# Performance work log

Hardware: AMD Instinct MI355X
Metric: run time of the kernel (lower is better)

## Reference

```python
import jax, jax.numpy as jnp
import numpy as np

WINSIZE = 11
SIGMA = 1.5
L_RANGE = 1.0

def _gaussian_window(winsize, channel, dtype=jnp.float32):
    x = jnp.arange(winsize, dtype=dtype)
    g = jnp.exp(-((x - winsize // 2) ** 2) / (2.0 * SIGMA ** 2))
    g = g / g.sum()
    w2d = jnp.outer(g, g)                      # [ws, ws]
    # depthwise kernel [channel, 1, ws, ws] (OIHW, feature_group_count=channel)
    return jnp.broadcast_to(w2d, (channel, 1, winsize, winsize))

def _dwconv(x, w, channel):
    pad = WINSIZE // 2
    return jax.lax.conv_general_dilated(
        x, w, window_strides=(1, 1), padding=[(pad, pad), (pad, pad)],
        dimension_numbers=('NCHW', 'OIHW', 'NCHW'),
        feature_group_count=channel)

def _ssim(X, Y):
    channel = X.shape[1]
    w = _gaussian_window(WINSIZE, channel, X.dtype)
    mu1 = _dwconv(X, w, channel)
    mu2 = _dwconv(Y, w, channel)
    mu1_sq = mu1 * mu1
    mu2_sq = mu2 * mu2
    mu1_mu2 = mu1 * mu2
    sigma1_sq = _dwconv(X * X, w, channel) - mu1_sq
    sigma2_sq = _dwconv(Y * Y, w, channel) - mu2_sq
    sigma12 = _dwconv(X * Y, w, channel) - mu1_mu2
    C1 = (0.01 * L_RANGE) ** 2
    C2 = (0.03 * L_RANGE) ** 2
    ssim_map = ((2.0 * mu1_mu2 + C1) * (2.0 * sigma12 + C2)) / \
               ((mu1_sq + mu2_sq + C1) * (sigma1_sq + sigma2_sq + C2))
    return jnp.mean(ssim_map)  # sizeavg=True

def setup_inputs() -> dict:
    key = jax.random.key(0)
    k1, k2 = jax.random.split(key)
    shape = (16, 3, 512, 512)
    X = jax.random.uniform(k1, shape, dtype=jnp.float32)
    Y = jax.random.uniform(k2, shape, dtype=jnp.float32)
    return {"X": X, "Y": Y}

def reference(X, Y):
    return 1.0 - _ssim(X, Y)
```

## Files before the change

### kernel.cpp

```cpp
#include <hip/hip_runtime.h>
#include <hip/hip_fp16.h>


#define ROWS 32
#define NI   (ROWS + 10)
#define NSTRIP 3072
#define NBLK  (NSTRIP / 4)
#define NPIX  12582912.0

static __device__ __forceinline__ unsigned fun16(unsigned hi, unsigned lo) {
    return (unsigned)((((unsigned long long)hi << 32) | lo) >> 16);
}
static __device__ __forceinline__ unsigned h2u(__half2 v) {
    unsigned u; __builtin_memcpy(&u, &v, 4); return u;
}
static __device__ __forceinline__ __half2 u2h(unsigned u) {
    __half2 v; __builtin_memcpy(&v, &u, 4); return v;
}

__global__ __launch_bounds__(256, 3) void ssim_sweep_kernel(
    const float* __restrict__ X, const float* __restrict__ Y,
    float* __restrict__ partial)
{
    __shared__ unsigned sbw[4][2][2][72];

    const int tid  = threadIdx.x;
    const int lane = tid & 63;
    const int w    = tid >> 6;
    const int sid  = blockIdx.x * 4 + w;
    const int img  = sid >> 6;
    const int rb   = (sid >> 2) & 15;
    const int cs   = (sid & 3) << 7;
    const int r0   = rb * ROWS;

    const float* __restrict__ Xi = X + (size_t)img * (512 * 512);
    const float* __restrict__ Yi = Y + (size_t)img * (512 * 512);

    float g[11];
    {
        float s = 0.f;
        #pragma unroll
        for (int i = 0; i < 11; ++i) {
            float d = (float)(i - 5);
            float e = expf(-d * d * (1.0f / 4.5f));
            g[i] = e; s += e;
        }
        float inv = 1.0f / s;
        #pragma unroll
        for (int i = 0; i < 11; ++i) g[i] *= inv;
    }
    __half2 w2[11];
    #pragma unroll
    for (int i = 0; i < 11; ++i) w2[i] = __float2half2_rn(g[i]);

    const int c2 = cs + 2 * lane;

    int hq = -1, hm = 0;
    if (lane >= 48 && lane < 54)      { hq = lane - 48; hm = 0; }
    else if (lane >= 56 && lane < 62) { hq = lane - 56; hm = 1; }
    const int  hwd = (hq < 0) ? 0 : (hq < 3 ? hq : 64 + hq);
    const int  hc  = cs - 6 + 2 * hwd;
    const bool hok = (hq >= 0) && ((unsigned)hc < 512u);
    const float* hbase = hm ? Yi : Xi;

    float2 nvx, nvy, nvh;
    #define STAGE_LOAD(J)                                                    \
        {                                                                    \
            int gr = r0 - 5 + (J);                                           \
            nvx = make_float2(0.f, 0.f); nvy = nvx; nvh = nvx;               \
            if ((unsigned)gr < 512u) {                                       \
                const float* xr = Xi + (size_t)gr * 512;                     \
                const float* yr = Yi + (size_t)gr * 512;                     \
                nvx = *(const float2*)(xr + c2);                             \
                nvy = *(const float2*)(yr + c2);                             \
                if (hok) nvh = *(const float2*)(hbase + (size_t)gr * 512 + hc); \
            }                                                                \
        }
    #define STAGE_WRITE(BUF)                                                 \
        {                                                                    \
            sbw[w][0][BUF][3 + lane] = h2u(__floats2half2_rn(nvx.x, nvx.y)); \
            sbw[w][1][BUF][3 + lane] = h2u(__floats2half2_rn(nvy.x, nvy.y)); \
            if (hq >= 0) sbw[w][hm][BUF][hwd] = h2u(__floats2half2_rn(nvh.x, nvh.y)); \
        }

    STAGE_LOAD(0);
    STAGE_WRITE(0);
    asm volatile("s_waitcnt lgkmcnt(0)" ::: "memory");

    __half2 ring[5][11];
    float acc = 0.f;
    const float C1 = 1e-4f, C2 = 9e-4f;
    const __half2 hz = __float2half2_rn(0.f);

    #pragma unroll 1
    for (int jb = 0; jb < 44; jb += 11) {
        #pragma unroll
        for (int ph = 0; ph < 11; ++ph) {
            const int j = jb + ph;
            if (j < NI) {
                const int cur = j & 1, nxt = cur ^ 1;

                if (j + 1 < NI) STAGE_LOAD(j + 1);

                unsigned Dx[7], Dy[7];
                #pragma unroll
                for (int k2 = 0; k2 < 7; ++k2) Dx[k2] = sbw[w][0][cur][lane + k2];
                #pragma unroll
                for (int k2 = 0; k2 < 7; ++k2) Dy[k2] = sbw[w][1][cur][lane + k2];

                __half2 hx = hz, hy = hz, hxx = hz, hyy = hz, hxy = hz;
                #pragma unroll
                for (int k = 0; k < 11; ++k) {
                    unsigned ux, uy;
                    if (k & 1) { ux = Dx[(k + 1) >> 1];            uy = Dy[(k + 1) >> 1]; }
                    else       { ux = fun16(Dx[(k >> 1) + 1], Dx[k >> 1]);
                                 uy = fun16(Dy[(k >> 1) + 1], Dy[k >> 1]); }
                    __half2 xk = u2h(ux), yk = u2h(uy);
                    __half2 wx = __hmul2(w2[k], xk);
                    __half2 wy = __hmul2(w2[k], yk);
                    hx  = __hadd2(hx, wx);
                    hy  = __hadd2(hy, wy);
                    hxx = __hfma2(wx, xk, hxx);
                    hyy = __hfma2(wy, yk, hyy);
                    hxy = __hfma2(wx, yk, hxy);
                }
                ring[0][ph] = hx;  ring[1][ph] = hy;
                ring[2][ph] = hxx; ring[3][ph] = hyy; ring[4][ph] = hxy;

                if (j >= 10) {
                    __half2 mu1 = hz, mu2 = hz, vxx = hz, vyy = hz, vxy = hz;
                    #pragma unroll
                    for (int k = 0; k < 11; ++k) {
                        const int s = (ph + 1 + k) % 11;
                        mu1 = __hfma2(w2[k], ring[0][s], mu1);
                        mu2 = __hfma2(w2[k], ring[1][s], mu2);
                        vxx = __hfma2(w2[k], ring[2][s], vxx);
                        vyy = __hfma2(w2[k], ring[3][s], vyy);
                        vxy = __hfma2(w2[k], ring[4][s], vxy);
                    }
                    float2 m1 = __half22float2(mu1);
                    float2 m2 = __half22float2(mu2);
                    float2 xx = __half22float2(vxx);
                    float2 yy = __half22float2(vyy);
                    float2 xy = __half22float2(vxy);
                    #pragma unroll
                    for (int h = 0; h < 2; ++h) {
                        float a1 = h ? m1.y : m1.x;
                        float a2 = h ? m2.y : m2.x;
                        float bx = h ? xx.y : xx.x;
                        float by = h ? yy.y : yy.x;
                        float bz = h ? xy.y : xy.x;
                        float m11 = a1 * a1, m22 = a2 * a2, m12 = a1 * a2;
                        float s1 = bx - m11, s2 = by - m22, s12 = bz - m12;
                        float num = (2.f * m12 + C1) * (2.f * s12 + C2);
                        float den = (m11 + m22 + C1) * (s1 + s2 + C2);
                        acc = fmaf(num, __builtin_amdgcn_rcpf(den), acc);
                    }
                }

                if (j + 1 < NI) STAGE_WRITE(nxt);
                asm volatile("s_waitcnt lgkmcnt(0)" ::: "memory");
            }
        }
    }

    #pragma unroll
    for (int off = 32; off > 0; off >>= 1)
        acc += __shfl_down(acc, off, 64);
    if (lane == 0) partial[sid] = acc;
}

__global__ __launch_bounds__(256) void ssim_reduce_kernel(
    const float* __restrict__ partial, float* __restrict__ out)
{
    const int tid = threadIdx.x;
    double s = 0.0;
    for (int i = tid; i < NSTRIP; i += 256) s += (double)partial[i];
    __shared__ double sd[256];
    sd[tid] = s;
    __syncthreads();
    for (int off = 128; off > 0; off >>= 1) {
        if (tid < off) sd[tid] += sd[tid + off];
        __syncthreads();
    }
    if (tid == 0) out[0] = (float)(1.0 - sd[0] / NPIX);
}

extern "C" void kernel_launch(void* const* d_in, const int* in_sizes, int n_in,
                              void* d_out, int out_size, void* d_ws, size_t ws_size,
                              hipStream_t stream) {
    const float* X = (const float*)d_in[0];
    const float* Y = (const float*)d_in[1];
    float* partial = (float*)d_ws;
    float* out = (float*)d_out;

    ssim_sweep_kernel<<<NBLK, 256, 0, stream>>>(X, Y, partial);
    ssim_reduce_kernel<<<1, 256, 0, stream>>>(partial, out);
}
```

Baseline: 61.19 us.

## Swap conv order to vertical-then-horizontal with wave shuffles instead of LDS

The separable Gaussian now runs vertically first over an 11-row register ring of raw X/Y values. The horizontal pass uses cross-lane shuffles, so the shared-memory staging buffers, halo-loading lanes and LDS waits are gone. Each wave covers overlapping 116-column strips with 6-column halos on each side, and a per-lane mask drops halo outputs. Strips are shorter (16 rows), which raises the vertical halo overhead and the number of redundant loads. Five shuffle-based horizontal convolutions per output row replace the previous LDS reads.

```diff
diff --git a/kernel.cpp b/kernel.cpp
--- a/kernel.cpp
+++ b/kernel.cpp
@@ -2,11 +2,11 @@
 #include <hip/hip_fp16.h>
 
 
-#define ROWS 32
-#define NI   (ROWS + 10)
-#define NSTRIP 3072
-#define NBLK  (NSTRIP / 4)
-#define NPIX  12582912.0
+#define R      16
+#define NIT    (R + 10)
+#define NSTRIP (48 * 32 * 5)
+#define NBLK   (NSTRIP / 4)
+#define NPIX   12582912.0
 
 static __device__ __forceinline__ unsigned fun16(unsigned hi, unsigned lo) {
     return (unsigned)((((unsigned long long)hi << 32) | lo) >> 16);
@@ -18,34 +18,35 @@
     __half2 v; __builtin_memcpy(&v, &u, 4); return v;
 }
 
-__global__ __launch_bounds__(256, 3) void ssim_sweep_kernel(
+__global__ __launch_bounds__(256) void ssim_vh_kernel(
     const float* __restrict__ X, const float* __restrict__ Y,
     float* __restrict__ partial)
 {
-    __shared__ unsigned sbw[4][2][2][72];
-
     const int tid  = threadIdx.x;
     const int lane = tid & 63;
     const int w    = tid >> 6;
     const int sid  = blockIdx.x * 4 + w;
-    const int img  = sid >> 6;
-    const int rb   = (sid >> 2) & 15;
-    const int cs   = (sid & 3) << 7;
-    const int r0   = rb * ROWS;
+    const int img  = sid / 160;
+    const int rem  = sid - img * 160;
+    const int band = rem / 5;
+    const int s    = rem - band * 5;
+    const int r0   = band * R;
+    const int oc   = 116 * s - 6;
+    const int c2   = oc + 2 * lane;
 
     const float* __restrict__ Xi = X + (size_t)img * (512 * 512);
     const float* __restrict__ Yi = Y + (size_t)img * (512 * 512);
 
     float g[11];
     {
-        float s = 0.f;
+        float sum = 0.f;
         #pragma unroll
         for (int i = 0; i < 11; ++i) {
             float d = (float)(i - 5);
             float e = expf(-d * d * (1.0f / 4.5f));
-            g[i] = e; s += e;
+            g[i] = e; sum += e;
         }
-        float inv = 1.0f / s;
+        float inv = 1.0f / sum;
         #pragma unroll
         for (int i = 0; i < 11; ++i) g[i] *= inv;
     }
@@ -53,113 +54,105 @@
     #pragma unroll
     for (int i = 0; i < 11; ++i) w2[i] = __float2half2_rn(g[i]);
 
-    const int c2 = cs + 2 * lane;
+    const bool  cok = ((unsigned)c2 < 512u);
+    const float msk = (lane >= 3 && lane <= 60 && cok) ? 1.f : 0.f;
 
-    int hq = -1, hm = 0;
-    if (lane >= 48 && lane < 54)      { hq = lane - 48; hm = 0; }
-    else if (lane >= 56 && lane < 62) { hq = lane - 56; hm = 1; }
-    const int  hwd = (hq < 0) ? 0 : (hq < 3 ? hq : 64 + hq);
-    const int  hc  = cs - 6 + 2 * hwd;
-    const bool hok = (hq >= 0) && ((unsigned)hc < 512u);
-    const float* hbase = hm ? Yi : Xi;
+    auto hconv = [&](__half2 vown) -> __half2 {
+        const unsigned W3  = h2u(vown);
+        const unsigned Wm3 = (unsigned)__shfl((int)W3, lane - 3, 64);
+        const unsigned Wm2 = (unsigned)__shfl((int)W3, lane - 2, 64);
+        const unsigned Wm1 = (unsigned)__shfl((int)W3, lane - 1, 64);
+        const unsigned Wp1 = (unsigned)__shfl((int)W3, lane + 1, 64);
+        const unsigned Wp2 = (unsigned)__shfl((int)W3, lane + 2, 64);
+        const unsigned Wp3 = (unsigned)__shfl((int)W3, lane + 3, 64);
+        __half2 h = __hmul2(w2[0], u2h(fun16(Wm2, Wm3)));
+        h = __hfma2(w2[1],  u2h(Wm2),            h);
+        h = __hfma2(w2[2],  u2h(fun16(Wm1, Wm2)), h);
+        h = __hfma2(w2[3],  u2h(Wm1),            h);
+        h = __hfma2(w2[4],  u2h(fun16(W3,  Wm1)), h);
+        h = __hfma2(w2[5],  vown,                h);
+        h = __hfma2(w2[6],  u2h(fun16(Wp1, W3)),  h);
+        h = __hfma2(w2[7],  u2h(Wp1),            h);
+        h = __hfma2(w2[8],  u2h(fun16(Wp2, Wp1)), h);
+        h = __hfma2(w2[9],  u2h(Wp2),            h);
+        h = __hfma2(w2[10], u2h(fun16(Wp3, Wp2)), h);
+        return h;
+    };
 
-    float2 nvx, nvy, nvh;
-    #define STAGE_LOAD(J)                                                    \
-        {                                                                    \
-            int gr = r0 - 5 + (J);                                           \
-            nvx = make_float2(0.f, 0.f); nvy = nvx; nvh = nvx;               \
-            if ((unsigned)gr < 512u) {                                       \
-                const float* xr = Xi + (size_t)gr * 512;                     \
-                const float* yr = Yi + (size_t)gr * 512;                     \
-                nvx = *(const float2*)(xr + c2);                             \
-                nvy = *(const float2*)(yr + c2);                             \
-                if (hok) nvh = *(const float2*)(hbase + (size_t)gr * 512 + hc); \
-            }                                                                \
+    float2 nx = make_float2(0.f, 0.f), ny = nx;
+    {
+        const int gr = r0 - 5;
+        if ((unsigned)gr < 512u && cok) {
+            nx = *(const float2*)(Xi + (size_t)gr * 512 + c2);
+            ny = *(const float2*)(Yi + (size_t)gr * 512 + c2);
         }
-    #define STAGE_WRITE(BUF)                                                 \
-        {                                                                    \
-            sbw[w][0][BUF][3 + lane] = h2u(__floats2half2_rn(nvx.x, nvx.y)); \
-            sbw[w][1][BUF][3 + lane] = h2u(__floats2half2_rn(nvy.x, nvy.y)); \
-            if (hq >= 0) sbw[w][hm][BUF][hwd] = h2u(__floats2half2_rn(nvh.x, nvh.y)); \
-        }
+    }
 
-    STAGE_LOAD(0);
-    STAGE_WRITE(0);
-    asm volatile("s_waitcnt lgkmcnt(0)" ::: "memory");
-
-    __half2 ring[5][11];
+    __half2 rx[11], ry[11];
     float acc = 0.f;
+    const __half2 hz = __float2half2_rn(0.f);
     const float C1 = 1e-4f, C2 = 9e-4f;
-    const __half2 hz = __float2half2_rn(0.f);
 
     #pragma unroll 1
-    for (int jb = 0; jb < 44; jb += 11) {
+    for (int jb = 0; jb < 33; jb += 11) {
         #pragma unroll
         for (int ph = 0; ph < 11; ++ph) {
             const int j = jb + ph;
-            if (j < NI) {
-                const int cur = j & 1, nxt = cur ^ 1;
+            if (j < NIT) {
+                rx[ph] = __floats2half2_rn(nx.x, nx.y);
+                ry[ph] = __floats2half2_rn(ny.x, ny.y);
 
-                if (j + 1 < NI) STAGE_LOAD(j + 1);
-
-                unsigned Dx[7], Dy[7];
-                #pragma unroll
-                for (int k2 = 0; k2 < 7; ++k2) Dx[k2] = sbw[w][0][cur][lane + k2];
-                #pragma unroll
-                for (int k2 = 0; k2 < 7; ++k2) Dy[k2] = sbw[w][1][cur][lane + k2];
-
-                __half2 hx = hz, hy = hz, hxx = hz, hyy = hz, hxy = hz;
-                #pragma unroll
-                for (int k = 0; k < 11; ++k) {
-                    unsigned ux, uy;
-                    if (k & 1) { ux = Dx[(k + 1) >> 1];            uy = Dy[(k + 1) >> 1]; }
-                    else       { ux = fun16(Dx[(k >> 1) + 1], Dx[k >> 1]);
-                                 uy = fun16(Dy[(k >> 1) + 1], Dy[k >> 1]); }
-                    __half2 xk = u2h(ux), yk = u2h(uy);
-                    __half2 wx = __hmul2(w2[k], xk);
-                    __half2 wy = __hmul2(w2[k], yk);
-                    hx  = __hadd2(hx, wx);
-                    hy  = __hadd2(hy, wy);
-                    hxx = __hfma2(wx, xk, hxx);
-                    hyy = __hfma2(wy, yk, hyy);
-                    hxy = __hfma2(wx, yk, hxy);
-                }
-                ring[0][ph] = hx;  ring[1][ph] = hy;
-                ring[2][ph] = hxx; ring[3][ph] = hyy; ring[4][ph] = hxy;
-
-                if (j >= 10) {
-                    __half2 mu1 = hz, mu2 = hz, vxx = hz, vyy = hz, vxy = hz;
-                    #pragma unroll
-                    for (int k = 0; k < 11; ++k) {
-                        const int s = (ph + 1 + k) % 11;
-                        mu1 = __hfma2(w2[k], ring[0][s], mu1);
-                        mu2 = __hfma2(w2[k], ring[1][s], mu2);
-                        vxx = __hfma2(w2[k], ring[2][s], vxx);
-                        vyy = __hfma2(w2[k], ring[3][s], vyy);
-                        vxy = __hfma2(w2[k], ring[4][s], vxy);
-                    }
-                    float2 m1 = __half22float2(mu1);
-                    float2 m2 = __half22float2(mu2);
-                    float2 xx = __half22float2(vxx);
-                    float2 yy = __half22float2(vyy);
-                    float2 xy = __half22float2(vxy);
-                    #pragma unroll
-                    for (int h = 0; h < 2; ++h) {
-                        float a1 = h ? m1.y : m1.x;
-                        float a2 = h ? m2.y : m2.x;
-                        float bx = h ? xx.y : xx.x;
-                        float by = h ? yy.y : yy.x;
-                        float bz = h ? xy.y : xy.x;
-                        float m11 = a1 * a1, m22 = a2 * a2, m12 = a1 * a2;
-                        float s1 = bx - m11, s2 = by - m22, s12 = bz - m12;
-                        float num = (2.f * m12 + C1) * (2.f * s12 + C2);
-                        float den = (m11 + m22 + C1) * (s1 + s2 + C2);
-                        acc = fmaf(num, __builtin_amdgcn_rcpf(den), acc);
+                if (j + 1 < NIT) {
+                    const int gr = r0 - 4 + j;
+                    nx = make_float2(0.f, 0.f); ny = nx;
+                    if ((unsigned)gr < 512u && cok) {
+                        nx = *(const float2*)(Xi + (size_t)gr * 512 + c2);
+                        ny = *(const float2*)(Yi + (size_t)gr * 512 + c2);
                     }
                 }
 
-                if (j + 1 < NI) STAGE_WRITE(nxt);
-                asm volatile("s_waitcnt lgkmcnt(0)" ::: "memory");
+                if (j >= 10) {
+                    __half2 vx = hz, vy = hz, vxx = hz, vyy = hz, vxy = hz;
+                    #pragma unroll
+                    for (int k = 0; k < 11; ++k) {
+                        const int sl = (ph + 1 + k) % 11;
+                        const __half2 xk = rx[sl], yk = ry[sl];
+                        const __half2 wx = __hmul2(w2[k], xk);
+                        const __half2 wy = __hmul2(w2[k], yk);
+                        vx  = __hadd2(vx, wx);
+                        vy  = __hadd2(vy, wy);
+                        vxx = __hfma2(wx, xk, vxx);
+                        vyy = __hfma2(wy, yk, vyy);
+                        vxy = __hfma2(wx, yk, vxy);
+                    }
+
+                    const __half2 hm1 = hconv(vx);
+                    const __half2 hm2 = hconv(vy);
+                    const __half2 hxx = hconv(vxx);
+                    const __half2 hyy = hconv(vyy);
+                    const __half2 hxy = hconv(vxy);
+
+                    const float2 m1 = __half22float2(hm1);
+                    const float2 m2 = __half22float2(hm2);
+                    const float2 xx = __half22float2(hxx);
+                    const float2 yy = __half22float2(hyy);
+                    const float2 xy = __half22float2(hxy);
+                    float val = 0.f;
+                    #pragma unroll
+                    for (int h = 0; h < 2; ++h) {
+                        const float a1 = h ? m1.y : m1.x;
+                        const float a2 = h ? m2.y : m2.x;
+                        const float bx = h ? xx.y : xx.x;
+                        const float by = h ? yy.y : yy.x;
+                        const float bz = h ? xy.y : xy.x;
+                        const float m11 = a1 * a1, m22 = a2 * a2, m12 = a1 * a2;
+                        const float s1 = bx - m11, s2 = by - m22, s12 = bz - m12;
+                        const float num = (2.f * m12 + C1) * (2.f * s12 + C2);
+                        const float den = (m11 + m22 + C1) * (s1 + s2 + C2);
+                        val = fmaf(num, __builtin_amdgcn_rcpf(den), val);
+                    }
+                    acc = fmaf(msk, val, acc);
+                }
             }
         }
     }
@@ -194,6 +187,6 @@
     float* partial = (float*)d_ws;
     float* out = (float*)d_out;
 
-    ssim_sweep_kernel<<<NBLK, 256, 0, stream>>>(X, Y, partial);
+    ssim_vh_kernel<<<NBLK, 256, 0, stream>>>(X, Y, partial);
     ssim_reduce_kernel<<<1, 256, 0, stream>>>(partial, out);
 }
```

Measured after the change: 79.89 us. 30.6% more time.
